# Kernel optimization log

Hardware: AMD Instinct MI355X
Metric: run time of the kernel (lower is better)

## Reference

```python
import jax, jax.numpy as jnp
import numpy as np

# norse default LIF/LI parameters
DT = 0.001
TAU_SYN_INV = 200.0   # 1 / 5e-3
TAU_MEM_INV = 100.0   # 1 / 1e-2
V_LEAK = 0.0
V_TH = 1.0
V_RESET = 0.0
ALPHA = 100.0          # SuperSpike surrogate slope ('super' method)

SEQ, BATCH, IN_F, HID, OUT_F = 512, 1024, 256, 512, 64


@jax.custom_vjp
def superspike(x):
    # forward: heaviside threshold; backward: SuperSpike surrogate
    return (x > 0).astype(x.dtype)

def _ss_fwd(x):
    return (x > 0).astype(x.dtype), x

def _ss_bwd(x, g):
    return (g / (ALPHA * jnp.abs(x) + 1.0) ** 2,)

superspike.defvjp(_ss_fwd, _ss_bwd)


def setup_inputs() -> dict:
    key = jax.random.key(0)
    kx, k1, k2, k3 = jax.random.split(key, 4)
    x = jax.random.normal(kx, (SEQ, BATCH, IN_F), dtype=jnp.float32)
    # norse LIFRecurrentCell init: randn * sqrt(2/hidden)
    w_in = jax.random.normal(k1, (HID, IN_F), dtype=jnp.float32) * np.sqrt(2.0 / HID)
    w_rec = jax.random.normal(k2, (HID, HID), dtype=jnp.float32) * np.sqrt(2.0 / HID)
    # fc_out: torch Linear default kaiming-uniform-ish; uniform(-1/sqrt(fan_in), 1/sqrt(fan_in))
    bound = 1.0 / np.sqrt(HID)
    w_out = jax.random.uniform(k3, (OUT_F, HID), dtype=jnp.float32, minval=-bound, maxval=bound)
    return {"x": x, "w_in": w_in, "w_rec": w_rec, "w_out": w_out}


def reference(x, w_in, w_rec, w_out):
    B = x.shape[1]
    H = w_in.shape[0]
    O = w_out.shape[0]

    def step(carry, x_t):
        z, v, i_syn, v_o, i_o = carry
        # LIF recurrent cell (norse lif_step with recurrent input)
        v_dec = v + DT * TAU_MEM_INV * ((V_LEAK - v) + i_syn)   # [B,H]
        i_dec = i_syn + DT * TAU_SYN_INV * (-i_syn)
        z_new = superspike(v_dec - V_TH)                         # spikes [B,H]
        v_new = (1.0 - z_new) * v_dec + z_new * V_RESET
        i_new = i_dec + x_t @ w_in.T + z @ w_rec.T
        # readout projection (no bias)
        y = z_new @ w_out.T                                      # [B,O]
        # LI cell (leaky integrator, feed-forward)
        vo_new = v_o + DT * TAU_MEM_INV * ((V_LEAK - v_o) + i_o)
        io_dec = i_o + DT * TAU_SYN_INV * (-i_o)
        io_new = io_dec + y
        return (z_new, v_new, i_new, vo_new, io_new), vo_new

    z0 = jnp.zeros((B, H), x.dtype)
    v0 = jnp.full((B, H), V_LEAK, x.dtype)
    i0 = jnp.zeros((B, H), x.dtype)
    vo0 = jnp.full((B, O), V_LEAK, x.dtype)
    io0 = jnp.zeros((B, O), x.dtype)
    _, voltages = jax.lax.scan(step, (z0, v0, i0, vo0, io0), x)
    return voltages  # [SEQ, B, O]
```

## Files before the change

### kernel.cpp

```cpp
#include <hip/hip_runtime.h>
#include <hip/hip_bf16.h>
#include <stdint.h>

#define SEQ   512
#define BATCH 1024
#define IN_F  256
#define HID   512
#define OUT_F 64

typedef float f32x2 __attribute__((ext_vector_type(2)));

static const size_t OFF_V   = 0;
static const size_t OFF_I   = 2097152;
static const size_t OFF_VO  = 4194304;
static const size_t OFF_IO  = 4456448;
static const size_t OFF_ZM  = 4718592;
static const size_t OFF_WRT = 4784128;
static const size_t OFF_WOT = 5834752;
static const size_t OFF_CUR = 5966080;

__global__ void init_state_kernel(float4* __restrict__ p, int n4) {
    int i = blockIdx.x * blockDim.x + threadIdx.x;
    int stride = gridDim.x * blockDim.x;
    float4 z = make_float4(0.f, 0.f, 0.f, 0.f);
    for (; i < n4; i += stride) p[i] = z;
}

__global__ void prep_kernel(const float* __restrict__ wrec, const float* __restrict__ wout,
                            float* __restrict__ wrecT, float* __restrict__ woutT) {
    int i = blockIdx.x * blockDim.x + threadIdx.x;
    int stride = gridDim.x * blockDim.x;
    for (int idx = i; idx < 513 * 512; idx += stride) {
        int j = idx >> 9, h = idx & 511;
        wrecT[idx] = (j < 512) ? wrec[h * 512 + j] : 0.0f;
    }
    for (int idx = i; idx < 513 * 64; idx += stride) {
        int h = idx >> 6, o = idx & 63;
        woutT[idx] = (h < 512) ? wout[o * 512 + h] : 0.0f;
    }
}

#define GBM 128
#define GBN 128
#define GBK 32
#define GLDK 132

__launch_bounds__(256)
__global__ void gemm_kernel(const float* __restrict__ A, const float* __restrict__ Bw,
                            float* __restrict__ C) {
    __shared__ float As[GBK][GLDK];
    __shared__ float Bs[GBK][GLDK];

    const int nwg = gridDim.x;
    const int cpx = nwg >> 3;
    const int logical = ((int)blockIdx.x & 7) * cpx + ((int)blockIdx.x >> 3);
    const int mb = logical >> 2;
    const int nb = logical & 3;

    const int t = threadIdx.x;
    const size_t m0 = (size_t)mb * GBM;
    const int n0 = nb * GBN;

    const int r  = t >> 1;
    const int kh = (t & 1) << 4;
    const float* Ap = A  + (m0 + (size_t)r) * IN_F + kh;
    const float* Bp = Bw + (size_t)(n0 + r) * IN_F + kh;

    const int tm = t >> 4;
    const int tn = t & 15;

    f32x2 acc[8][4] = {};

    for (int k0 = 0; k0 < IN_F; k0 += GBK) {
        float4 a0 = *(const float4*)(Ap + k0);
        float4 a1 = *(const float4*)(Ap + k0 + 4);
        float4 a2 = *(const float4*)(Ap + k0 + 8);
        float4 a3 = *(const float4*)(Ap + k0 + 12);
        float4 b0 = *(const float4*)(Bp + k0);
        float4 b1 = *(const float4*)(Bp + k0 + 4);
        float4 b2 = *(const float4*)(Bp + k0 + 8);
        float4 b3 = *(const float4*)(Bp + k0 + 12);
        __syncthreads();
        {
            float av[16], bv[16];
            *(float4*)(av + 0) = a0; *(float4*)(av + 4)  = a1;
            *(float4*)(av + 8) = a2; *(float4*)(av + 12) = a3;
            *(float4*)(bv + 0) = b0; *(float4*)(bv + 4)  = b1;
            *(float4*)(bv + 8) = b2; *(float4*)(bv + 12) = b3;
            #pragma unroll
            for (int i = 0; i < 16; ++i) {
                As[kh + i][r] = av[i];
                Bs[kh + i][r] = bv[i];
            }
        }
        __syncthreads();
        #pragma unroll
        for (int k = 0; k < GBK; ++k) {
            float am[8], bn[8];
            *(float4*)(am + 0) = *(const float4*)&As[k][tm * 8];
            *(float4*)(am + 4) = *(const float4*)&As[k][tm * 8 + 4];
            *(float4*)(bn + 0) = *(const float4*)&Bs[k][tn * 8];
            *(float4*)(bn + 4) = *(const float4*)&Bs[k][tn * 8 + 4];
            f32x2 bp0 = { bn[0], bn[1] }, bp1 = { bn[2], bn[3] };
            f32x2 bp2 = { bn[4], bn[5] }, bp3 = { bn[6], bn[7] };
            #pragma unroll
            for (int rr = 0; rr < 8; ++rr) {
                f32x2 ar = { am[rr], am[rr] };
                acc[rr][0] = __builtin_elementwise_fma(ar, bp0, acc[rr][0]);
                acc[rr][1] = __builtin_elementwise_fma(ar, bp1, acc[rr][1]);
                acc[rr][2] = __builtin_elementwise_fma(ar, bp2, acc[rr][2]);
                acc[rr][3] = __builtin_elementwise_fma(ar, bp3, acc[rr][3]);
            }
        }
    }
    #pragma unroll
    for (int rr = 0; rr < 8; ++rr) {
        float* Cp = C + (m0 + (size_t)(tm * 8 + rr)) * HID + n0 + tn * 8;
        float4 c0 = make_float4(acc[rr][0][0], acc[rr][0][1], acc[rr][1][0], acc[rr][1][1]);
        float4 c1 = make_float4(acc[rr][2][0], acc[rr][2][1], acc[rr][3][0], acc[rr][3][1]);
        *(float4*)(Cp + 0) = c0;
        *(float4*)(Cp + 4) = c1;
    }
}

__launch_bounds__(512, 8)
__global__ void rec_kernel(const float* __restrict__ cur,
                           const float* __restrict__ wrecT,
                           const float* __restrict__ woutT,
                           float* __restrict__ stV, float* __restrict__ stI,
                           float* __restrict__ stVO, float* __restrict__ stIO,
                           unsigned long long* __restrict__ stZM,
                           float* __restrict__ out, int t0, int csteps) {
    __shared__ __attribute__((aligned(16))) unsigned short slist[2][528];
    __shared__ unsigned long long zm[8];
    __shared__ float ypart[8][64];

    const int b = blockIdx.x;
    const int tid = threadIdx.x;
    const int lane = tid & 63;
    const int w = tid >> 6;
    const int t4 = tid << 2;
    const int l4 = lane << 2;

    const char* __restrict__ wrecB = (const char*)wrecT;
    const char* __restrict__ woutB = (const char*)woutT;

    float v  = stV[b * HID + tid];
    float ii = stI[b * HID + tid];
    float vo = 0.f, io = 0.f;
    if (tid < OUT_F) { vo = stVO[b * OUT_F + tid]; io = stIO[b * OUT_F + tid]; }
    if (tid < 8) zm[tid] = stZM[b * 8 + tid];
    __syncthreads();

    int cnt, cpad;
    {
        unsigned long long mm[8];
        #pragma unroll
        for (int q = 0; q < 8; ++q) mm[q] = zm[q];
        int pre = 0, total = 0;
        #pragma unroll
        for (int q = 0; q < 8; ++q) { int pc = (int)__popcll(mm[q]); total += pc; if (q < w) pre += pc; }
        int below = (int)__popcll(mm[w] & ((1ull << lane) - 1ull));
        if ((mm[w] >> lane) & 1ull) slist[0][pre + below] = (unsigned short)tid;
        cnt = total; cpad = (cnt + 7) & ~7;
        if (tid < 8 && cnt + tid < cpad) slist[0][cnt + tid] = (unsigned short)HID;
    }
    __syncthreads();

    const float* __restrict__ curRow  = cur + (size_t)b * HID;
    const size_t step_stride = (size_t)BATCH * HID;

    float curv = curRow[tid];
    int cb = 0;
    for (int tl = 0; tl < csteps; ++tl) {
        float cur_nxt = 0.f;
        if (tl + 1 < csteps) {
            curRow += step_stride;
            cur_nxt = curRow[tid];
        }

        float rec = 0.f;
        for (int k = 0; k < cpad; k += 8) {
            uint4 pk = *(const uint4*)&slist[cb][k];
            int o0 = ((pk.x & 0xffff) << 11) | t4;
            int o1 = ((pk.x >> 16) << 11) | t4;
            int o2 = ((pk.y & 0xffff) << 11) | t4;
            int o3 = ((pk.y >> 16) << 11) | t4;
            int o4 = ((pk.z & 0xffff) << 11) | t4;
            int o5 = ((pk.z >> 16) << 11) | t4;
            int o6 = ((pk.w & 0xffff) << 11) | t4;
            int o7 = ((pk.w >> 16) << 11) | t4;
            rec += *(const float*)(wrecB + o0);
            rec += *(const float*)(wrecB + o1);
            rec += *(const float*)(wrecB + o2);
            rec += *(const float*)(wrecB + o3);
            rec += *(const float*)(wrecB + o4);
            rec += *(const float*)(wrecB + o5);
            rec += *(const float*)(wrecB + o6);
            rec += *(const float*)(wrecB + o7);
        }
        float vdec = v + 0.1f * ((0.0f - v) + ii);
        int spike = (vdec > 1.0f) ? 1 : 0;
        v = spike ? 0.0f : vdec;
        float idec = ii + 0.2f * (0.0f - ii);
        ii = (idec + curv) + rec;
        curv = cur_nxt;

        unsigned long long m = __ballot(spike);
        if (lane == 0) zm[w] = m;
        __syncthreads();
        {
            unsigned long long mq[8];
            #pragma unroll
            for (int q = 0; q < 8; ++q) mq[q] = zm[q];
            int pre = 0, total = 0;
            #pragma unroll
            for (int q = 0; q < 8; ++q) { int pc = (int)__popcll(mq[q]); total += pc; if (q < w) pre += pc; }
            int below = (int)__popcll(mq[w] & ((1ull << lane) - 1ull));
            if ((mq[w] >> lane) & 1ull) slist[cb ^ 1][pre + below] = (unsigned short)tid;
            cnt = total; cpad = (cnt + 7) & ~7;
            if (tid < 8 && cnt + tid < cpad) slist[cb ^ 1][cnt + tid] = (unsigned short)HID;
        }
        __syncthreads();
        {
            float yp = 0.f;
            for (int k = w; k < cnt; k += 8) {
                int hh = slist[cb ^ 1][k];
                yp += *(const float*)(woutB + ((hh << 8) | l4));
            }
            ypart[w][lane] = yp;
        }
        __syncthreads();
        if (tid < OUT_F) {
            float y = 0.f;
            #pragma unroll
            for (int q = 0; q < 8; ++q) y += ypart[q][tid];
            float von = vo + 0.1f * ((0.0f - vo) + io);
            float iodec = io + 0.2f * (0.0f - io);
            io = iodec + y;
            vo = von;
            out[(((size_t)(t0 + tl)) * BATCH + b) * OUT_F + tid] = von;
        }
        cb ^= 1;
    }
    stV[b * HID + tid] = v;
    stI[b * HID + tid] = ii;
    if (tid < OUT_F) { stVO[b * OUT_F + tid] = vo; stIO[b * OUT_F + tid] = io; }
    if (tid < 8) stZM[b * 8 + tid] = zm[tid];
}

extern "C" void kernel_launch(void* const* d_in, const int* in_sizes, int n_in,
                              void* d_out, int out_size, void* d_ws, size_t ws_size,
                              hipStream_t stream) {
    const float* x     = (const float*)d_in[0];
    const float* w_in  = (const float*)d_in[1];
    const float* w_rec = (const float*)d_in[2];
    const float* w_out = (const float*)d_in[3];
    float* out = (float*)d_out;
    char* ws = (char*)d_ws;

    float* stV  = (float*)(ws + OFF_V);
    float* stI  = (float*)(ws + OFF_I);
    float* stVO = (float*)(ws + OFF_VO);
    float* stIO = (float*)(ws + OFF_IO);
    unsigned long long* stZM = (unsigned long long*)(ws + OFF_ZM);
    float* wrecT = (float*)(ws + OFF_WRT);
    float* woutT = (float*)(ws + OFF_WOT);
    float* curbuf = (float*)(ws + OFF_CUR);

    size_t cap = (ws_size > OFF_CUR) ? (ws_size - OFF_CUR) : 0;
    int csteps = 1;
    for (int c = 512; c >= 1; c >>= 1) {
        if ((size_t)c * (size_t)BATCH * HID * 4 <= cap) { csteps = c; break; }
    }

    {
        int n4 = (int)(OFF_WRT / 16);
        int blocks = (n4 + 255) / 256;
        if (blocks > 4096) blocks = 4096;
        hipLaunchKernelGGL(init_state_kernel, dim3(blocks), dim3(256), 0, stream,
                           (float4*)ws, n4);
    }
    hipLaunchKernelGGL(prep_kernel, dim3(512), dim3(256), 0, stream,
                       w_rec, w_out, wrecT, woutT);

    for (int t0 = 0; t0 < SEQ; t0 += csteps) {
        hipLaunchKernelGGL(gemm_kernel, dim3(csteps * 32), dim3(256), 0, stream,
                           x + (size_t)t0 * BATCH * IN_F, w_in, curbuf);
        hipLaunchKernelGGL(rec_kernel, dim3(BATCH), dim3(512), 0, stream,
                           curbuf, wrecT, woutT, stV, stI, stVO, stIO, stZM, out, t0, csteps);
    }
}
```

Before: 2.997 ms.

## Pack recurrent weights as float2 pairs, halve rec block size, prefetch GEMM tiles

```diff
diff --git a/kernel.cpp b/kernel.cpp
--- a/kernel.cpp
+++ b/kernel.cpp
@@ -27,12 +27,17 @@
 }
 
 __global__ void prep_kernel(const float* __restrict__ wrec, const float* __restrict__ wout,
-                            float* __restrict__ wrecT, float* __restrict__ woutT) {
+                            float2* __restrict__ pw, float* __restrict__ woutT) {
     int i = blockIdx.x * blockDim.x + threadIdx.x;
     int stride = gridDim.x * blockDim.x;
-    for (int idx = i; idx < 513 * 512; idx += stride) {
-        int j = idx >> 9, h = idx & 511;
-        wrecT[idx] = (j < 512) ? wrec[h * 512 + j] : 0.0f;
+    for (int idx = i; idx < 513 * 256; idx += stride) {
+        int j = idx >> 8, h2 = idx & 255;
+        float2 v = make_float2(0.f, 0.f);
+        if (j < 512) {
+            v.x = wrec[h2 * 512 + j];
+            v.y = wrec[(h2 + 256) * 512 + j];
+        }
+        pw[idx] = v;
     }
     for (int idx = i; idx < 513 * 64; idx += stride) {
         int h = idx >> 6, o = idx & 63;
@@ -71,15 +76,16 @@
 
     f32x2 acc[8][4] = {};
 
+    float4 a0 = *(const float4*)(Ap + 0);
+    float4 a1 = *(const float4*)(Ap + 4);
+    float4 a2 = *(const float4*)(Ap + 8);
+    float4 a3 = *(const float4*)(Ap + 12);
+    float4 b0 = *(const float4*)(Bp + 0);
+    float4 b1 = *(const float4*)(Bp + 4);
+    float4 b2 = *(const float4*)(Bp + 8);
+    float4 b3 = *(const float4*)(Bp + 12);
+
     for (int k0 = 0; k0 < IN_F; k0 += GBK) {
-        float4 a0 = *(const float4*)(Ap + k0);
-        float4 a1 = *(const float4*)(Ap + k0 + 4);
-        float4 a2 = *(const float4*)(Ap + k0 + 8);
-        float4 a3 = *(const float4*)(Ap + k0 + 12);
-        float4 b0 = *(const float4*)(Bp + k0);
-        float4 b1 = *(const float4*)(Bp + k0 + 4);
-        float4 b2 = *(const float4*)(Bp + k0 + 8);
-        float4 b3 = *(const float4*)(Bp + k0 + 12);
         __syncthreads();
         {
             float av[16], bv[16];
@@ -94,6 +100,17 @@
             }
         }
         __syncthreads();
+        if (k0 + GBK < IN_F) {
+            const int kn = k0 + GBK;
+            a0 = *(const float4*)(Ap + kn);
+            a1 = *(const float4*)(Ap + kn + 4);
+            a2 = *(const float4*)(Ap + kn + 8);
+            a3 = *(const float4*)(Ap + kn + 12);
+            b0 = *(const float4*)(Bp + kn);
+            b1 = *(const float4*)(Bp + kn + 4);
+            b2 = *(const float4*)(Bp + kn + 8);
+            b3 = *(const float4*)(Bp + kn + 12);
+        }
         #pragma unroll
         for (int k = 0; k < GBK; ++k) {
             float am[8], bn[8];
@@ -123,9 +140,9 @@
     }
 }
 
-__launch_bounds__(512, 8)
+__launch_bounds__(256, 4)
 __global__ void rec_kernel(const float* __restrict__ cur,
-                           const float* __restrict__ wrecT,
+                           const float2* __restrict__ pw,
                            const float* __restrict__ woutT,
                            float* __restrict__ stV, float* __restrict__ stI,
                            float* __restrict__ stVO, float* __restrict__ stIO,
@@ -133,20 +150,22 @@
                            float* __restrict__ out, int t0, int csteps) {
     __shared__ __attribute__((aligned(16))) unsigned short slist[2][528];
     __shared__ unsigned long long zm[8];
-    __shared__ float ypart[8][64];
+    __shared__ float ypart[4][64];
 
     const int b = blockIdx.x;
     const int tid = threadIdx.x;
     const int lane = tid & 63;
     const int w = tid >> 6;
-    const int t4 = tid << 2;
+    const int t8 = tid << 3;
     const int l4 = lane << 2;
 
-    const char* __restrict__ wrecB = (const char*)wrecT;
+    const char* __restrict__ pwB   = (const char*)pw;
     const char* __restrict__ woutB = (const char*)woutT;
 
-    float v  = stV[b * HID + tid];
-    float ii = stI[b * HID + tid];
+    float v0 = stV[b * HID + tid];
+    float v1 = stV[b * HID + 256 + tid];
+    float i0 = stI[b * HID + tid];
+    float i1 = stI[b * HID + 256 + tid];
     float vo = 0.f, io = 0.f;
     if (tid < OUT_F) { vo = stVO[b * OUT_F + tid]; io = stIO[b * OUT_F + tid]; }
     if (tid < 8) zm[tid] = stZM[b * 8 + tid];
@@ -157,74 +176,102 @@
         unsigned long long mm[8];
         #pragma unroll
         for (int q = 0; q < 8; ++q) mm[q] = zm[q];
-        int pre = 0, total = 0;
+        int pc[8], total = 0;
         #pragma unroll
-        for (int q = 0; q < 8; ++q) { int pc = (int)__popcll(mm[q]); total += pc; if (q < w) pre += pc; }
-        int below = (int)__popcll(mm[w] & ((1ull << lane) - 1ull));
-        if ((mm[w] >> lane) & 1ull) slist[0][pre + below] = (unsigned short)tid;
+        for (int q = 0; q < 8; ++q) { pc[q] = (int)__popcll(mm[q]); total += pc[q]; }
+        unsigned long long lmask = (1ull << lane) - 1ull;
+        int pre0 = 0, pre1 = 0;
+        #pragma unroll
+        for (int q = 0; q < 8; ++q) { if (q < w) pre0 += pc[q]; if (q < w + 4) pre1 += pc[q]; }
+        if ((mm[w] >> lane) & 1ull)
+            slist[0][pre0 + (int)__popcll(mm[w] & lmask)] = (unsigned short)tid;
+        if ((mm[w + 4] >> lane) & 1ull)
+            slist[0][pre1 + (int)__popcll(mm[w + 4] & lmask)] = (unsigned short)(256 + tid);
         cnt = total; cpad = (cnt + 7) & ~7;
         if (tid < 8 && cnt + tid < cpad) slist[0][cnt + tid] = (unsigned short)HID;
     }
     __syncthreads();
 
-    const float* __restrict__ curRow  = cur + (size_t)b * HID;
+    const float* __restrict__ curRow = cur + (size_t)b * HID;
     const size_t step_stride = (size_t)BATCH * HID;
 
-    float curv = curRow[tid];
+    float c0v = curRow[tid];
+    float c1v = curRow[256 + tid];
     int cb = 0;
     for (int tl = 0; tl < csteps; ++tl) {
-        float cur_nxt = 0.f;
+        float c0n = 0.f, c1n = 0.f;
         if (tl + 1 < csteps) {
             curRow += step_stride;
-            cur_nxt = curRow[tid];
-        }
-
-        float rec = 0.f;
+            c0n = curRow[tid];
+            c1n = curRow[256 + tid];
+        }
+
+        float rec0 = 0.f, rec1 = 0.f;
         for (int k = 0; k < cpad; k += 8) {
             uint4 pk = *(const uint4*)&slist[cb][k];
-            int o0 = ((pk.x & 0xffff) << 11) | t4;
-            int o1 = ((pk.x >> 16) << 11) | t4;
-            int o2 = ((pk.y & 0xffff) << 11) | t4;
-            int o3 = ((pk.y >> 16) << 11) | t4;
-            int o4 = ((pk.z & 0xffff) << 11) | t4;
-            int o5 = ((pk.z >> 16) << 11) | t4;
-            int o6 = ((pk.w & 0xffff) << 11) | t4;
-            int o7 = ((pk.w >> 16) << 11) | t4;
-            rec += *(const float*)(wrecB + o0);
-            rec += *(const float*)(wrecB + o1);
-            rec += *(const float*)(wrecB + o2);
-            rec += *(const float*)(wrecB + o3);
-            rec += *(const float*)(wrecB + o4);
-            rec += *(const float*)(wrecB + o5);
-            rec += *(const float*)(wrecB + o6);
-            rec += *(const float*)(wrecB + o7);
-        }
-        float vdec = v + 0.1f * ((0.0f - v) + ii);
-        int spike = (vdec > 1.0f) ? 1 : 0;
-        v = spike ? 0.0f : vdec;
-        float idec = ii + 0.2f * (0.0f - ii);
-        ii = (idec + curv) + rec;
-        curv = cur_nxt;
-
-        unsigned long long m = __ballot(spike);
-        if (lane == 0) zm[w] = m;
+            int o0 = ((pk.x & 0xffff) << 11) | t8;
+            int o1 = ((pk.x >> 16) << 11) | t8;
+            int o2 = ((pk.y & 0xffff) << 11) | t8;
+            int o3 = ((pk.y >> 16) << 11) | t8;
+            int o4 = ((pk.z & 0xffff) << 11) | t8;
+            int o5 = ((pk.z >> 16) << 11) | t8;
+            int o6 = ((pk.w & 0xffff) << 11) | t8;
+            int o7 = ((pk.w >> 16) << 11) | t8;
+            float2 g0 = *(const float2*)(pwB + o0);
+            float2 g1 = *(const float2*)(pwB + o1);
+            float2 g2 = *(const float2*)(pwB + o2);
+            float2 g3 = *(const float2*)(pwB + o3);
+            float2 g4 = *(const float2*)(pwB + o4);
+            float2 g5 = *(const float2*)(pwB + o5);
+            float2 g6 = *(const float2*)(pwB + o6);
+            float2 g7 = *(const float2*)(pwB + o7);
+            rec0 += g0.x; rec1 += g0.y;
+            rec0 += g1.x; rec1 += g1.y;
+            rec0 += g2.x; rec1 += g2.y;
+            rec0 += g3.x; rec1 += g3.y;
+            rec0 += g4.x; rec1 += g4.y;
+            rec0 += g5.x; rec1 += g5.y;
+            rec0 += g6.x; rec1 += g6.y;
+            rec0 += g7.x; rec1 += g7.y;
+        }
+        float vd0 = v0 + 0.1f * ((0.0f - v0) + i0);
+        float vd1 = v1 + 0.1f * ((0.0f - v1) + i1);
+        int s0 = (vd0 > 1.0f) ? 1 : 0;
+        int s1 = (vd1 > 1.0f) ? 1 : 0;
+        v0 = s0 ? 0.0f : vd0;
+        v1 = s1 ? 0.0f : vd1;
+        float id0 = i0 + 0.2f * (0.0f - i0);
+        float id1 = i1 + 0.2f * (0.0f - i1);
+        i0 = (id0 + c0v) + rec0;
+        i1 = (id1 + c1v) + rec1;
+        c0v = c0n; c1v = c1n;
+
+        unsigned long long m0 = __ballot(s0);
+        unsigned long long m1 = __ballot(s1);
+        if (lane == 0) { zm[w] = m0; zm[w + 4] = m1; }
         __syncthreads();
         {
             unsigned long long mq[8];
             #pragma unroll
             for (int q = 0; q < 8; ++q) mq[q] = zm[q];
-            int pre = 0, total = 0;
-            #pragma unroll
-            for (int q = 0; q < 8; ++q) { int pc = (int)__popcll(mq[q]); total += pc; if (q < w) pre += pc; }
-            int below = (int)__popcll(mq[w] & ((1ull << lane) - 1ull));
-            if ((mq[w] >> lane) & 1ull) slist[cb ^ 1][pre + below] = (unsigned short)tid;
+            int pc[8], total = 0;
+            #pragma unroll
+            for (int q = 0; q < 8; ++q) { pc[q] = (int)__popcll(mq[q]); total += pc[q]; }
+            unsigned long long lmask = (1ull << lane) - 1ull;
+            int pre0 = 0, pre1 = 0;
+            #pragma unroll
+            for (int q = 0; q < 8; ++q) { if (q < w) pre0 += pc[q]; if (q < w + 4) pre1 += pc[q]; }
+            if ((mq[w] >> lane) & 1ull)
+                slist[cb ^ 1][pre0 + (int)__popcll(mq[w] & lmask)] = (unsigned short)tid;
+            if ((mq[w + 4] >> lane) & 1ull)
+                slist[cb ^ 1][pre1 + (int)__popcll(mq[w + 4] & lmask)] = (unsigned short)(256 + tid);
             cnt = total; cpad = (cnt + 7) & ~7;
             if (tid < 8 && cnt + tid < cpad) slist[cb ^ 1][cnt + tid] = (unsigned short)HID;
         }
         __syncthreads();
         {
             float yp = 0.f;
-            for (int k = w; k < cnt; k += 8) {
+            for (int k = w; k < cnt; k += 4) {
                 int hh = slist[cb ^ 1][k];
                 yp += *(const float*)(woutB + ((hh << 8) | l4));
             }
@@ -232,9 +279,7 @@
         }
         __syncthreads();
         if (tid < OUT_F) {
-            float y = 0.f;
-            #pragma unroll
-            for (int q = 0; q < 8; ++q) y += ypart[q][tid];
+            float y = ((ypart[0][tid] + ypart[1][tid]) + ypart[2][tid]) + ypart[3][tid];
             float von = vo + 0.1f * ((0.0f - vo) + io);
             float iodec = io + 0.2f * (0.0f - io);
             io = iodec + y;
@@ -243,8 +288,10 @@
         }
         cb ^= 1;
     }
-    stV[b * HID + tid] = v;
-    stI[b * HID + tid] = ii;
+    stV[b * HID + tid] = v0;
+    stV[b * HID + 256 + tid] = v1;
+    stI[b * HID + tid] = i0;
+    stI[b * HID + 256 + tid] = i1;
     if (tid < OUT_F) { stVO[b * OUT_F + tid] = vo; stIO[b * OUT_F + tid] = io; }
     if (tid < 8) stZM[b * 8 + tid] = zm[tid];
 }
@@ -264,7 +311,7 @@
     float* stVO = (float*)(ws + OFF_VO);
     float* stIO = (float*)(ws + OFF_IO);
     unsigned long long* stZM = (unsigned long long*)(ws + OFF_ZM);
-    float* wrecT = (float*)(ws + OFF_WRT);
+    float2* pw   = (float2*)(ws + OFF_WRT);
     float* woutT = (float*)(ws + OFF_WOT);
     float* curbuf = (float*)(ws + OFF_CUR);
 
@@ -282,12 +329,12 @@
                            (float4*)ws, n4);
     }
     hipLaunchKernelGGL(prep_kernel, dim3(512), dim3(256), 0, stream,
-                       w_rec, w_out, wrecT, woutT);
+                       w_rec, w_out, pw, woutT);
 
     for (int t0 = 0; t0 < SEQ; t0 += csteps) {
         hipLaunchKernelGGL(gemm_kernel, dim3(csteps * 32), dim3(256), 0, stream,
                            x + (size_t)t0 * BATCH * IN_F, w_in, curbuf);
-        hipLaunchKernelGGL(rec_kernel, dim3(BATCH), dim3(512), 0, stream,
-                           curbuf, wrecT, woutT, stV, stI, stVO, stIO, stZM, out, t0, csteps);
-    }
-}
+        hipLaunchKernelGGL(rec_kernel, dim3(BATCH), dim3(256), 0, stream,
+                           curbuf, pw, woutT, stV, stI, stVO, stIO, stZM, out, t0, csteps);
+    }
+}
```

Measured after the change: 3.359 ms. +12.1%, slower.
